# Kernel optimization log

Hardware: AMD Instinct MI355X
Metric: run time of the kernel (lower is better)

The kernel has to match this reference:

```python
import jax, jax.numpy as jnp
import numpy as np

GRID_SIZE = 5
SPLINE_ORDER = 3
GRID_RANGE = (-1.0, 1.0)
NUM_BASIS = GRID_SIZE + SPLINE_ORDER  # 8


def setup_inputs() -> dict:
    key = jax.random.key(0)
    k1, k2 = jax.random.split(key)
    x = jax.random.normal(k1, (16, 256, 256, 32), dtype=jnp.float32)
    bound = GRID_RANGE[1] - GRID_RANGE[0]
    grid = jnp.linspace(
        GRID_RANGE[0] - SPLINE_ORDER * bound / GRID_SIZE,
        GRID_RANGE[1] + SPLINE_ORDER * bound / GRID_SIZE,
        GRID_SIZE + 2 * SPLINE_ORDER + 1,
    ).astype(jnp.float32)  # [12], matches tf.linspace(-2.2, 2.2, 12)
    # Per-channel Dense(1, use_bias=False) weights stacked: [in_channel, num_basis]
    W = jax.random.normal(k2, (32, NUM_BASIS), dtype=jnp.float32) * 0.1
    return {"x": x, "grid": grid, "W": W}


def _spline_bases(x, grid, spline_order):
    # Cox-de Boor recursion, basis axis kept last: [..., C, len(grid)-1-order]
    xg = x[..., None]  # [B,H,W,C,1]
    bases = ((xg >= grid[:-1]) & (xg < grid[1:])).astype(x.dtype)  # order-0
    for k in range(1, spline_order + 1):
        left = (xg - grid[:-(k + 1)]) / (grid[k:-1] - grid[:-(k + 1)]) * bases[..., :-1]
        right = (grid[k + 1:] - xg) / (grid[k + 1:] - grid[1:-k]) * bases[..., 1:]
        bases = left + right
    return bases  # [B,H,W,C, grid_size+spline_order]


def reference(x, grid, W):
    bases = _spline_bases(x, grid, SPLINE_ORDER)  # [B,H,W,C,K]
    # Per-channel Dense(1): contract basis axis with channel-specific weights.
    return jnp.einsum('...ck,ck->...c', bases, W)  # [B,H,W,C]
```

## Files before the change

kernel.cpp:

```cpp
#include <hip/hip_runtime.h>


#define NCH 32
#define NINT 11

typedef float vf4 __attribute__((ext_vector_type(4)));

__global__ __launch_bounds__(256) void kan_bspline_kernel(
    const float* __restrict__ x,
    const float* __restrict__ grid,
    const float* __restrict__ W,
    float* __restrict__ out,
    int n4) {
  __shared__ float4 coef[NCH * NINT + 8];

  const int tid = blockIdx.x * blockDim.x + threadIdx.x;
  const vf4* __restrict__ x4 = (const vf4*)x;

  vf4 xv = (tid < n4) ? x4[tid] : (vf4)(0.0f);

  const float sixth = 1.0f / 6.0f;
  for (int e = threadIdx.x; e < NCH * NINT; e += 256) {
    int c = e / NINT;
    int i = e - c * NINT;
    float w[4];
#pragma unroll
    for (int k = 0; k < 4; ++k) {
      int j = i - 3 + k;
      w[k] = (j >= 0 && j < 8) ? W[c * 8 + j] : 0.0f;
    }
    float4 a;
    a.x = (w[0] + 4.0f * w[1] + w[2]) * sixth;
    a.y = 0.5f * (w[2] - w[0]);
    a.z = 0.5f * (w[0] - 2.0f * w[1] + w[2]);
    a.w = (w[3] - w[0]) * sixth + 0.5f * (w[1] - w[2]);
    coef[e + (c >> 2)] = a;
  }
  __syncthreads();

  if (tid >= n4) return;

  const float g0 = grid[0];
  const float inv_h = 11.0f / (grid[11] - grid[0]);

  const int c0 = (4 * tid) & 31;
  int base[4];
#pragma unroll
  for (int k = 0; k < 4; ++k) base[k] = (c0 + k) * NINT + (c0 >> 2);

  float xs[4] = {xv.x, xv.y, xv.z, xv.w};
  float rs[4];
#pragma unroll
  for (int k = 0; k < 4; ++k) {
    float u = (xs[k] - g0) * inv_h;
    float fi = floorf(u);
    float fic = fminf(fmaxf(fi, 0.0f), 10.0f);
    float t = u - fic;
    int i = (int)fic;
    float4 a = coef[base[k] + i];
    float r = fmaf(fmaf(fmaf(a.w, t, a.z), t, a.y), t, a.x);
    rs[k] = (fi >= 0.0f && fi <= 10.0f) ? r : 0.0f;
  }

  vf4 ov;
  ov.x = rs[0]; ov.y = rs[1]; ov.z = rs[2]; ov.w = rs[3];
  vf4* __restrict__ o4 = (vf4*)out;
  __builtin_nontemporal_store(ov, &o4[tid]);
}

extern "C" void kernel_launch(void* const* d_in, const int* in_sizes, int n_in,
                              void* d_out, int out_size, void* d_ws, size_t ws_size,
                              hipStream_t stream) {
  const float* x    = (const float*)d_in[0];
  const float* grid = (const float*)d_in[1];
  const float* W    = (const float*)d_in[2];
  float* out        = (float*)d_out;

  const int n  = in_sizes[0];
  const int n4 = n / 4;

  const int threads = 256;
  const int blocks  = (n4 + threads - 1) / threads;
  hipLaunchKernelGGL(kan_bspline_kernel, dim3(blocks), dim3(threads), 0, stream,
                     x, grid, W, out, n4);
}
```

Measured before the change: 229.5 us.

## Process eight float4 per thread with fixed grid and batched loads

Launches a fixed 4096 blocks, and each thread handles eight float4 elements at grid-stride offsets. All eight loads are issued before any compute to keep more memory requests in flight. The per-block coefficient-table setup is now amortized over more elements, and W is staged through shared memory first. Bounds checks are removed and the launch now assumes n4 equals 4096*256*8 exactly (true for the test shape), so other sizes would go out of bounds or leave outputs unwritten.

```diff
diff --git a/kernel.cpp b/kernel.cpp
--- a/kernel.cpp
+++ b/kernel.cpp
@@ -6,28 +6,28 @@
 
 typedef float vf4 __attribute__((ext_vector_type(4)));
 
-__global__ __launch_bounds__(256) void kan_bspline_kernel(
+__global__ __launch_bounds__(256, 8) void kan_bspline_kernel(
     const float* __restrict__ x,
     const float* __restrict__ grid,
     const float* __restrict__ W,
     float* __restrict__ out,
     int n4) {
+  __shared__ float wsh[NCH * 8];
   __shared__ float4 coef[NCH * NINT + 8];
 
-  const int tid = blockIdx.x * blockDim.x + threadIdx.x;
-  const vf4* __restrict__ x4 = (const vf4*)x;
-
-  vf4 xv = (tid < n4) ? x4[tid] : (vf4)(0.0f);
+  const int tl = threadIdx.x;
+  wsh[tl] = W[tl];
+  __syncthreads();
 
   const float sixth = 1.0f / 6.0f;
-  for (int e = threadIdx.x; e < NCH * NINT; e += 256) {
+  for (int e = tl; e < NCH * NINT; e += 256) {
     int c = e / NINT;
     int i = e - c * NINT;
     float w[4];
 #pragma unroll
     for (int k = 0; k < 4; ++k) {
       int j = i - 3 + k;
-      w[k] = (j >= 0 && j < 8) ? W[c * 8 + j] : 0.0f;
+      w[k] = (j >= 0 && j < 8) ? wsh[c * 8 + j] : 0.0f;
     }
     float4 a;
     a.x = (w[0] + 4.0f * w[1] + w[2]) * sixth;
@@ -38,34 +38,55 @@
   }
   __syncthreads();
 
-  if (tid >= n4) return;
-
   const float g0 = grid[0];
   const float inv_h = 11.0f / (grid[11] - grid[0]);
 
+  const int tid = blockIdx.x * blockDim.x + tl;
+  const int S = gridDim.x * blockDim.x;
   const int c0 = (4 * tid) & 31;
   int base[4];
 #pragma unroll
   for (int k = 0; k < 4; ++k) base[k] = (c0 + k) * NINT + (c0 >> 2);
 
-  float xs[4] = {xv.x, xv.y, xv.z, xv.w};
-  float rs[4];
+  const vf4* __restrict__ x4 = (const vf4*)x;
+  vf4* __restrict__ o4 = (vf4*)out;
+
+  vf4 xa[4], xb[4];
 #pragma unroll
-  for (int k = 0; k < 4; ++k) {
-    float u = (xs[k] - g0) * inv_h;
-    float fi = floorf(u);
-    float fic = fminf(fmaxf(fi, 0.0f), 10.0f);
-    float t = u - fic;
-    int i = (int)fic;
-    float4 a = coef[base[k] + i];
-    float r = fmaf(fmaf(fmaf(a.w, t, a.z), t, a.y), t, a.x);
-    rs[k] = (fi >= 0.0f && fi <= 10.0f) ? r : 0.0f;
+  for (int j = 0; j < 4; ++j) xa[j] = x4[tid + j * S];
+#pragma unroll
+  for (int j = 0; j < 4; ++j) xb[j] = x4[tid + (4 + j) * S];
+
+#define PROC(xv, ov)                                               \
+  {                                                                \
+    float xs_[4] = {(xv).x, (xv).y, (xv).z, (xv).w};               \
+    float rs_[4];                                                  \
+    _Pragma("unroll") for (int k = 0; k < 4; ++k) {                \
+      float u = (xs_[k] - g0) * inv_h;                             \
+      float fi = floorf(u);                                        \
+      float fic = fminf(fmaxf(fi, 0.0f), 10.0f);                   \
+      float t = u - fic;                                           \
+      int i = (int)fic;                                            \
+      float4 a = coef[base[k] + i];                                \
+      float r = fmaf(fmaf(fmaf(a.w, t, a.z), t, a.y), t, a.x);     \
+      rs_[k] = (fi >= 0.0f && fi <= 10.0f) ? r : 0.0f;             \
+    }                                                              \
+    (ov).x = rs_[0]; (ov).y = rs_[1]; (ov).z = rs_[2]; (ov).w = rs_[3]; \
   }
 
-  vf4 ov;
-  ov.x = rs[0]; ov.y = rs[1]; ov.z = rs[2]; ov.w = rs[3];
-  vf4* __restrict__ o4 = (vf4*)out;
-  __builtin_nontemporal_store(ov, &o4[tid]);
+#pragma unroll
+  for (int j = 0; j < 4; ++j) {
+    vf4 ov;
+    PROC(xa[j], ov);
+    __builtin_nontemporal_store(ov, &o4[tid + j * S]);
+  }
+#pragma unroll
+  for (int j = 0; j < 4; ++j) {
+    vf4 ov;
+    PROC(xb[j], ov);
+    __builtin_nontemporal_store(ov, &o4[tid + (4 + j) * S]);
+  }
+#undef PROC
 }
 
 extern "C" void kernel_launch(void* const* d_in, const int* in_sizes, int n_in,
@@ -80,7 +101,7 @@
   const int n4 = n / 4;
 
   const int threads = 256;
-  const int blocks  = (n4 + threads - 1) / threads;
+  const int blocks  = 4096;
   hipLaunchKernelGGL(kan_bspline_kernel, dim3(blocks), dim3(threads), 0, stream,
                      x, grid, W, out, n4);
 }
```

Measured after the change: 247.0 us. 1.08x slower.

## Precompute cubic coefficient table in setup kernel and copy into LDS per block

Applied to the files above, without the earlier changes.

Splits the per-block coefficient derivation out into a single-block setup kernel that writes a 352-entry float4 table to workspace. The main kernel then just copies that table into shared memory instead of recomputing it in every block. The table is also re-laid out so that lanes with different channel groups index consecutive entries, which is meant to reduce LDS bank conflicts. The cost is an extra kernel launch, plus a global read of the table in every block.

```diff
diff --git a/kernel.cpp b/kernel.cpp
--- a/kernel.cpp
+++ b/kernel.cpp
@@ -3,24 +3,14 @@
 
 #define NCH 32
 #define NINT 11
+#define TBL 352
 
 typedef float vf4 __attribute__((ext_vector_type(4)));
 
-__global__ __launch_bounds__(256) void kan_bspline_kernel(
-    const float* __restrict__ x,
-    const float* __restrict__ grid,
-    const float* __restrict__ W,
-    float* __restrict__ out,
-    int n4) {
-  __shared__ float4 coef[NCH * NINT + 8];
-
-  const int tid = blockIdx.x * blockDim.x + threadIdx.x;
-  const vf4* __restrict__ x4 = (const vf4*)x;
-
-  vf4 xv = (tid < n4) ? x4[tid] : (vf4)(0.0f);
-
+__global__ __launch_bounds__(256) void kan_setup(const float* __restrict__ W,
+                                                 float4* __restrict__ tbl) {
   const float sixth = 1.0f / 6.0f;
-  for (int e = threadIdx.x; e < NCH * NINT; e += 256) {
+  for (int e = threadIdx.x; e < TBL; e += 256) {
     int c = e / NINT;
     int i = e - c * NINT;
     float w[4];
@@ -34,8 +24,26 @@
     a.y = 0.5f * (w[2] - w[0]);
     a.z = 0.5f * (w[0] - 2.0f * w[1] + w[2]);
     a.w = (w[3] - w[0]) * sixth + 0.5f * (w[1] - w[2]);
-    coef[e + (c >> 2)] = a;
+    int es = (c >> 2) + 8 * ((c & 3) * NINT + i);
+    tbl[es] = a;
   }
+}
+
+__global__ __launch_bounds__(256) void kan_main(const float* __restrict__ x,
+                                                const float* __restrict__ grid,
+                                                const float4* __restrict__ tbl,
+                                                float* __restrict__ out,
+                                                int n4) {
+  __shared__ float4 coef[TBL];
+
+  const int tl = threadIdx.x;
+  const int tid = blockIdx.x * blockDim.x + tl;
+  const vf4* __restrict__ x4 = (const vf4*)x;
+
+  vf4 xv = (tid < n4) ? x4[tid] : (vf4)(0.0f);
+
+  coef[tl] = tbl[tl];
+  if (tl + 256 < TBL) coef[tl + 256] = tbl[tl + 256];
   __syncthreads();
 
   if (tid >= n4) return;
@@ -43,10 +51,7 @@
   const float g0 = grid[0];
   const float inv_h = 11.0f / (grid[11] - grid[0]);
 
-  const int c0 = (4 * tid) & 31;
-  int base[4];
-#pragma unroll
-  for (int k = 0; k < 4; ++k) base[k] = (c0 + k) * NINT + (c0 >> 2);
+  const int g = tid & 7;
 
   float xs[4] = {xv.x, xv.y, xv.z, xv.w};
   float rs[4];
@@ -57,15 +62,14 @@
     float fic = fminf(fmaxf(fi, 0.0f), 10.0f);
     float t = u - fic;
     int i = (int)fic;
-    float4 a = coef[base[k] + i];
+    float4 a = coef[g + 88 * k + 8 * i];
     float r = fmaf(fmaf(fmaf(a.w, t, a.z), t, a.y), t, a.x);
     rs[k] = (fi >= 0.0f && fi <= 10.0f) ? r : 0.0f;
   }
 
   vf4 ov;
   ov.x = rs[0]; ov.y = rs[1]; ov.z = rs[2]; ov.w = rs[3];
-  vf4* __restrict__ o4 = (vf4*)out;
-  __builtin_nontemporal_store(ov, &o4[tid]);
+  __builtin_nontemporal_store(ov, &((vf4*)out)[tid]);
 }
 
 extern "C" void kernel_launch(void* const* d_in, const int* in_sizes, int n_in,
@@ -75,12 +79,15 @@
   const float* grid = (const float*)d_in[1];
   const float* W    = (const float*)d_in[2];
   float* out        = (float*)d_out;
+  float4* tbl       = (float4*)d_ws;
 
   const int n  = in_sizes[0];
   const int n4 = n / 4;
 
+  hipLaunchKernelGGL(kan_setup, dim3(1), dim3(256), 0, stream, W, tbl);
+
   const int threads = 256;
   const int blocks  = (n4 + threads - 1) / threads;
-  hipLaunchKernelGGL(kan_bspline_kernel, dim3(blocks), dim3(threads), 0, stream,
-                     x, grid, W, out, n4);
+  hipLaunchKernelGGL(kan_main, dim3(blocks), dim3(threads), 0, stream,
+                     x, grid, tbl, out, n4);
 }
```

Result: no change. 227.2 us (-1.0%).
